# Kernel optimization log

Hardware: AMD Instinct MI355X
Metric: run time of the kernel (lower is better)

## Reference

```python
import jax, jax.numpy as jnp
import numpy as np

N = 50000
E = 800000
F_IN = 128
HEADS = 4
C_OUT = 32
NEG_SLOPE = 0.2


def setup_inputs() -> dict:
    key = jax.random.key(0)
    k_x, k_e, k_w, k_as, k_ad, k_b = jax.random.split(key, 6)
    x = jax.random.normal(k_x, (N, F_IN), dtype=jnp.float32)
    edge_index = jax.random.randint(k_e, (2, E), 0, N, dtype=jnp.int32)
    # Glorot-style init for linear weight [F_IN, HEADS*C_OUT] and attention vectors.
    scale_w = 1.0 / np.sqrt(F_IN)
    W = jax.random.normal(k_w, (F_IN, HEADS * C_OUT), dtype=jnp.float32) * scale_w
    scale_a = 1.0 / np.sqrt(C_OUT)
    att_src = jax.random.normal(k_as, (HEADS, C_OUT), dtype=jnp.float32) * scale_a
    att_dst = jax.random.normal(k_ad, (HEADS, C_OUT), dtype=jnp.float32) * scale_a
    bias = jnp.zeros((HEADS * C_OUT,), dtype=jnp.float32)
    return {"x": x, "edge_index": edge_index, "W": W, "att_src": att_src,
            "att_dst": att_dst, "bias": bias}


def reference(x, edge_index, W, att_src, att_dst, bias):
    n = x.shape[0]
    # add self loops (PyG add_self_loops=True)
    loops = jnp.arange(n, dtype=edge_index.dtype)
    src = jnp.concatenate([edge_index[0], loops])  # [E+N]
    dst = jnp.concatenate([edge_index[1], loops])  # [E+N]
    edge_index_full = jnp.stack([src, dst])

    h = (x @ W).reshape(n, HEADS, C_OUT)           # [N,H,C]
    a_src = jnp.einsum('nhc,hc->nh', h, att_src)   # [N,H]
    a_dst = jnp.einsum('nhc,hc->nh', h, att_dst)   # [N,H]

    e = jax.nn.leaky_relu(a_src[src] + a_dst[dst], NEG_SLOPE)  # [E',H]
    # segment softmax over edges grouped by destination node
    m = jax.ops.segment_max(e, dst, num_segments=n)            # [N,H]
    e = jnp.exp(e - m[dst])
    s = jax.ops.segment_sum(e, dst, num_segments=n)            # [N,H]
    alpha = e / (s[dst] + 1e-16)                               # [E',H]

    msg = h[src] * alpha[:, :, None]                           # [E',H,C]
    out = jax.ops.segment_sum(msg, dst, num_segments=n)        # [N,H,C]
    out = out.reshape(n, HEADS * C_OUT) + bias                 # concat=True
    return out, edge_index_full, alpha
```

## Files before the change

kernel.cpp:

```cpp
#include <hip/hip_runtime.h>

#define NNODES 50000
#define NEDGES 800000
#define ETOT   (NEDGES + NNODES)
#define FIN    128
#define FOUT   128
#define HEADS  4
#define NEG    0.2f
#define RCAP   64
#define WSTR   136
#define NBUCK  196
#define CAPB   4608

typedef float  f32x4 __attribute__((ext_vector_type(4)));
typedef int    i32x4 __attribute__((ext_vector_type(4)));
typedef short  s16x8 __attribute__((ext_vector_type(8)));
typedef unsigned short u16x8 __attribute__((ext_vector_type(8)));

__device__ __forceinline__ float lrelu(float v) { return v > 0.f ? v : NEG * v; }
__device__ __forceinline__ float4 e4(float4 a, float4 b) {
    return make_float4(__expf(lrelu(a.x + b.x)), __expf(lrelu(a.y + b.y)),
                       __expf(lrelu(a.z + b.z)), __expf(lrelu(a.w + b.w)));
}
__device__ __forceinline__ unsigned short f2bf(float f) {
    unsigned u = __float_as_uint(f);
    return (unsigned short)((u + 0x7FFFu + ((u >> 16) & 1u)) >> 16);
}
__device__ __forceinline__ void nt_store4(float* p, float a, float b, float c, float d) {
    f32x4 v = {a, b, c, d};
    __builtin_nontemporal_store(v, (f32x4*)p);
}

__global__ __launch_bounds__(256) void k_wt(const float* __restrict__ W,
                                            unsigned short* __restrict__ Wt,
                                            int* __restrict__ gcnt)
{
    if (blockIdx.x == 0 && threadIdx.x < NBUCK) gcnt[threadIdx.x] = 0;
    const int i = blockIdx.x * 256 + threadIdx.x;
    const int c = i & 127, kq = i >> 7;
    const int k0 = kq * 4;
    ushort4 v;
    v.x = f2bf(W[(k0 + 0) * 128 + c]);
    v.y = f2bf(W[(k0 + 1) * 128 + c]);
    v.z = f2bf(W[(k0 + 2) * 128 + c]);
    v.w = f2bf(W[(k0 + 3) * 128 + c]);
    *(ushort4*)(Wt + c * 128 + k0) = v;
}

__global__ __launch_bounds__(256) void k_gemm(
    const float* __restrict__ x, const unsigned short* __restrict__ Wtg,
    const float* __restrict__ att_s, const float* __restrict__ att_d,
    unsigned short* __restrict__ hb, float* __restrict__ a_src, float* __restrict__ a_dst)
{
    __shared__ unsigned short Wl[128 * WSTR];
    __shared__ unsigned short Xl[64 * WSTR];

    const int tid = threadIdx.x;
    const int nbase = blockIdx.x * 64;

    for (int i = tid; i < 2048; i += 256) {
        int c = i >> 4, q = i & 15;
        *(u16x8*)(&Wl[c * WSTR + q * 8]) = *(const u16x8*)(&Wtg[c * 128 + q * 8]);
    }
#pragma unroll
    for (int it = 0; it < 8; it++) {
        int flat = it * 256 + tid;
        int row = flat >> 5, kq = flat & 31;
        int gn = nbase + row; if (gn >= NNODES) gn = NNODES - 1;
        float4 v = *(const float4*)(x + (size_t)gn * FIN + kq * 4);
        ushort4 b;
        b.x = f2bf(v.x); b.y = f2bf(v.y); b.z = f2bf(v.z); b.w = f2bf(v.w);
        *(ushort4*)(&Xl[row * WSTR + kq * 4]) = b;
    }
    __syncthreads();

    const int wid = tid >> 6, lane = tid & 63;
    const int r16 = lane & 15;
    const int kg  = lane >> 4;

    s16x8 af[4];
#pragma unroll
    for (int t = 0; t < 4; t++)
        af[t] = *(const s16x8*)(&Xl[(wid * 16 + r16) * WSTR + t * 32 + kg * 8]);

    float pa[4] = {0.f, 0.f, 0.f, 0.f};
    float pd[4] = {0.f, 0.f, 0.f, 0.f};

#pragma unroll
    for (int cg = 0; cg < 8; cg++) {
        s16x8 bf[4];
#pragma unroll
        for (int t = 0; t < 4; t++)
            bf[t] = *(const s16x8*)(&Wl[(cg * 16 + r16) * WSTR + t * 32 + kg * 8]);
        f32x4 acc = {0.f, 0.f, 0.f, 0.f};
#pragma unroll
        for (int t = 0; t < 4; t++)
            acc = __builtin_amdgcn_mfma_f32_16x16x32_bf16(af[t], bf[t], acc, 0, 0, 0);

        const int col = cg * 16 + r16;
        const float asv = att_s[col], adv = att_d[col];
#pragma unroll
        for (int i2 = 0; i2 < 4; i2++) {
            int node = nbase + wid * 16 + kg * 4 + i2;
            if (node < NNODES)
                hb[(size_t)node * FOUT + col] = f2bf(acc[i2]);
            pa[i2] = fmaf(acc[i2], asv, pa[i2]);
            pd[i2] = fmaf(acc[i2], adv, pd[i2]);
        }
        if (cg & 1) {
            const int head = cg >> 1;
#pragma unroll
            for (int i2 = 0; i2 < 4; i2++) {
                float a = pa[i2], d = pd[i2];
                a += __shfl_xor(a, 1); a += __shfl_xor(a, 2);
                a += __shfl_xor(a, 4); a += __shfl_xor(a, 8);
                d += __shfl_xor(d, 1); d += __shfl_xor(d, 2);
                d += __shfl_xor(d, 4); d += __shfl_xor(d, 8);
                if (r16 == 0) {
                    int node = nbase + wid * 16 + kg * 4 + i2;
                    if (node < NNODES) {
                        a_src[node * HEADS + head] = a;
                        a_dst[node * HEADS + head] = d;
                    }
                }
                pa[i2] = 0.f; pd[i2] = 0.f;
            }
        }
    }
}

__global__ __launch_bounds__(256) void k_bin(
    const int* __restrict__ ei, int* __restrict__ gcnt, unsigned* __restrict__ region)
{
    __shared__ int lcnt[256], lofs[256], gbase[256], lpos[256], scan[256];
    __shared__ unsigned recs[4096];
    const int tid = threadIdx.x;
    const int q0 = blockIdx.x * 1024;

    lcnt[tid] = 0;
    __syncthreads();

    i32x4 sq[4], dq[4];
    bool v[4];
#pragma unroll
    for (int j = 0; j < 4; j++) {
        const int q = q0 + tid + j * 256;
        v[j] = (q < NEDGES / 4);
        const int qi = v[j] ? q : 0;
        sq[j] = ((const i32x4*)ei)[qi];
        dq[j] = ((const i32x4*)(ei + NEDGES))[qi];
    }
#pragma unroll
    for (int j = 0; j < 4; j++)
        if (v[j]) {
#pragma unroll
            for (int c = 0; c < 4; c++) atomicAdd(&lcnt[dq[j][c] >> 8], 1);
        }
    __syncthreads();
    scan[tid] = lcnt[tid];
    __syncthreads();
    for (int o = 1; o < 256; o <<= 1) {
        int t = (tid >= o) ? scan[tid - o] : 0;
        __syncthreads();
        scan[tid] += t;
        __syncthreads();
    }
    lofs[tid] = scan[tid] - lcnt[tid];
    if (tid < NBUCK) gbase[tid] = atomicAdd(&gcnt[tid], lcnt[tid]);
    lpos[tid] = 0;
    __syncthreads();
#pragma unroll
    for (int j = 0; j < 4; j++)
        if (v[j]) {
#pragma unroll
            for (int c = 0; c < 4; c++) {
                const int d = dq[j][c], b = d >> 8;
                const int idx = lofs[b] + atomicAdd(&lpos[b], 1);
                recs[idx] = (unsigned)sq[j][c] | ((unsigned)d << 16);
            }
        }
    __syncthreads();
    const int m = scan[255];
    for (int i = tid; i < m; i += 256) {
        const unsigned rec = recs[i];
        const int b = rec >> 24;
        const int off = gbase[b] + (i - lofs[b]);
        if (off < CAPB) region[(size_t)b * CAPB + off] = rec;
    }
}

__global__ __launch_bounds__(256) void k_asm(
    const unsigned* __restrict__ region, const int* __restrict__ gcnt,
    int* __restrict__ cnt, unsigned short* __restrict__ csr16)
{
    __shared__ unsigned short rows[256 * RCAP];
    __shared__ int lcnt[256];
    const int tid = threadIdx.x;
    const int b = blockIdx.x;
    lcnt[tid] = 0;
    __syncthreads();

    const int m = min(gcnt[b], CAPB);
    for (int i = tid; i < m; i += 256) {
        const unsigned u = region[(size_t)b * CAPB + i];
        const int dl = (u >> 16) & 255;
        const int sl = atomicAdd(&lcnt[dl], 1);
        if (sl < RCAP) rows[dl * RCAP + sl] = (unsigned short)(u & 0xFFFFu);
    }
    __syncthreads();

    const int nodebase = b * 256;
    const int nrows = min(256, NNODES - nodebase);
    for (int i = tid; i < nrows * 8; i += 256) {
        const int r = i >> 3, q = i & 7;
        *(u16x8*)(&csr16[((size_t)(nodebase + r) << 6) + q * 8]) =
            *(const u16x8*)(&rows[r * RCAP + q * 8]);
    }
    if (tid < nrows) cnt[nodebase + tid] = lcnt[tid];
}

__global__ __launch_bounds__(256) void k_msg(
    const unsigned short* __restrict__ hb, const float* __restrict__ a_src,
    const float* __restrict__ a_dst, const int* __restrict__ cnt,
    const unsigned short* __restrict__ csr16, const float* __restrict__ bias,
    float* __restrict__ out, float* __restrict__ nd)
{
    const int tid = threadIdx.x;
    const int wid = tid >> 6, lane = tid & 63;
    const int n = blockIdx.x * 4 + wid;
    __shared__ unsigned short slds[4][RCAP];
    __shared__ float elds[4][RCAP * 4];

    const int deg_r = min(cnt[n], RCAP - 1);
    const int deg = deg_r + 1;
    const float4 ad = ((const float4*)a_dst)[n];

    unsigned s = (unsigned)n;
    float4 ev = make_float4(0.f, 0.f, 0.f, 0.f);
    if (lane < deg) {
        if (lane < deg_r) s = csr16[(n << 6) + lane];
        float4 as = ((const float4*)a_src)[s];
        ev = e4(as, ad);
    }
    float4 den = ev;
#pragma unroll
    for (int o = 32; o >= 1; o >>= 1) {
        den.x += __shfl_xor(den.x, o);
        den.y += __shfl_xor(den.y, o);
        den.z += __shfl_xor(den.z, o);
        den.w += __shfl_xor(den.w, o);
    }
    const float4 inv = make_float4(1.f / (den.x + 1e-16f), 1.f / (den.y + 1e-16f),
                                   1.f / (den.z + 1e-16f), 1.f / (den.w + 1e-16f));
    if (lane == 0) {
        ((float4*)nd)[n * 2]     = ad;
        ((float4*)nd)[n * 2 + 1] = inv;
    }
    slds[wid][lane] = (unsigned short)s;
    ((float4*)elds[wid])[lane] =
        make_float4(ev.x * inv.x, ev.y * inv.y, ev.z * inv.z, ev.w * inv.w);

    const int sub = lane >> 4;
    const int c8  = lane & 15;
    const int head = c8 >> 2;
    const char* hbase = (const char*)hb;
    float acc[8];
#pragma unroll
    for (int j = 0; j < 8; j++) acc[j] = 0.f;
    const int dp = (deg + 3) & ~3;

    int i0 = sub;
    float al = elds[wid][i0 * 4 + head];
    unsigned si = slds[wid][i0];
    float4 u = *(const float4*)(hbase + si * 256u + c8 * 16u);

    for (int base = 4; base < dp; base += 4) {
        const int i1 = base + sub;
        const float al2 = elds[wid][i1 * 4 + head];
        const unsigned si2 = slds[wid][i1];
        const float4 u2 = *(const float4*)(hbase + si2 * 256u + c8 * 16u);

        const unsigned w0 = __float_as_uint(u.x), w1 = __float_as_uint(u.y);
        const unsigned w2 = __float_as_uint(u.z), w3 = __float_as_uint(u.w);
        acc[0] = fmaf(__uint_as_float(w0 << 16),          al, acc[0]);
        acc[1] = fmaf(__uint_as_float(w0 & 0xFFFF0000u),  al, acc[1]);
        acc[2] = fmaf(__uint_as_float(w1 << 16),          al, acc[2]);
        acc[3] = fmaf(__uint_as_float(w1 & 0xFFFF0000u),  al, acc[3]);
        acc[4] = fmaf(__uint_as_float(w2 << 16),          al, acc[4]);
        acc[5] = fmaf(__uint_as_float(w2 & 0xFFFF0000u),  al, acc[5]);
        acc[6] = fmaf(__uint_as_float(w3 << 16),          al, acc[6]);
        acc[7] = fmaf(__uint_as_float(w3 & 0xFFFF0000u),  al, acc[7]);

        u = u2; al = al2;
    }
    {
        const unsigned w0 = __float_as_uint(u.x), w1 = __float_as_uint(u.y);
        const unsigned w2 = __float_as_uint(u.z), w3 = __float_as_uint(u.w);
        acc[0] = fmaf(__uint_as_float(w0 << 16),          al, acc[0]);
        acc[1] = fmaf(__uint_as_float(w0 & 0xFFFF0000u),  al, acc[1]);
        acc[2] = fmaf(__uint_as_float(w1 << 16),          al, acc[2]);
        acc[3] = fmaf(__uint_as_float(w1 & 0xFFFF0000u),  al, acc[3]);
        acc[4] = fmaf(__uint_as_float(w2 << 16),          al, acc[4]);
        acc[5] = fmaf(__uint_as_float(w2 & 0xFFFF0000u),  al, acc[5]);
        acc[6] = fmaf(__uint_as_float(w3 << 16),          al, acc[6]);
        acc[7] = fmaf(__uint_as_float(w3 & 0xFFFF0000u),  al, acc[7]);
    }
#pragma unroll
    for (int j = 0; j < 8; j++) {
        acc[j] += __shfl_xor(acc[j], 16);
        acc[j] += __shfl_xor(acc[j], 32);
    }
    if (lane < 16) {
        const float4 b0 = ((const float4*)bias)[c8 * 2];
        const float4 b1 = ((const float4*)bias)[c8 * 2 + 1];
        ((float4*)out)[(size_t)n * 32 + c8 * 2] =
            make_float4(acc[0] + b0.x, acc[1] + b0.y, acc[2] + b0.z, acc[3] + b0.w);
        ((float4*)out)[(size_t)n * 32 + c8 * 2 + 1] =
            make_float4(acc[4] + b1.x, acc[5] + b1.y, acc[6] + b1.z, acc[7] + b1.w);
    }
}

__global__ __launch_bounds__(256) void k_alpha(
    const int* __restrict__ ei, const float* __restrict__ a_src,
    const float* __restrict__ nd, float* __restrict__ alpha,
    float* __restrict__ out_edge)
{
    const int i4 = blockIdx.x * blockDim.x + threadIdx.x;
    if (i4 >= ETOT / 4) return;
    i32x4 s4, d4;
    if (i4 < NEDGES / 4) {
        s4 = __builtin_nontemporal_load(&((const i32x4*)ei)[i4]);
        d4 = __builtin_nontemporal_load(&((const i32x4*)ei)[NEDGES / 4 + i4]);
    } else {
        const int n0 = i4 * 4 - NEDGES;
        s4 = d4 = (i32x4){n0, n0 + 1, n0 + 2, n0 + 3};
    }
    nt_store4(out_edge + (size_t)i4 * 4,
              (float)s4.x, (float)s4.y, (float)s4.z, (float)s4.w);
    nt_store4(out_edge + (size_t)(ETOT / 4 + i4) * 4,
              (float)d4.x, (float)d4.y, (float)d4.z, (float)d4.w);

    const float4* as4p = (const float4*)a_src;
    const float4* nd4p = (const float4*)nd;
#pragma unroll
    for (int j = 0; j < 4; j++) {
        const int s = s4[j];
        const int d = d4[j];
        float4 as = as4p[s];
        float4 ad = nd4p[d * 2];
        float4 iv = nd4p[d * 2 + 1];
        float4 ev = e4(as, ad);
        nt_store4(alpha + ((size_t)i4 * 4 + j) * 4,
                  ev.x * iv.x, ev.y * iv.y, ev.z * iv.z, ev.w * iv.w);
    }
}

extern "C" void kernel_launch(void* const* d_in, const int* in_sizes, int n_in,
                              void* d_out, int out_size, void* d_ws, size_t ws_size,
                              hipStream_t stream)
{
    const float* x     = (const float*)d_in[0];
    const int*   ei    = (const int*)  d_in[1];
    const float* W     = (const float*)d_in[2];
    const float* att_s = (const float*)d_in[3];
    const float* att_d = (const float*)d_in[4];
    const float* bias  = (const float*)d_in[5];

    unsigned short* hb = (unsigned short*)d_ws;
    float* a_src  = (float*)(hb + (size_t)NNODES * FOUT);
    float* a_dst  = a_src + NNODES * HEADS;
    float* nd     = a_dst + NNODES * HEADS;
    int*   cnt    = (int*)(nd + (size_t)NNODES * 8);
    unsigned short* csr16 = (unsigned short*)(cnt + NNODES);
    unsigned short* wt    = csr16 + (size_t)NNODES * RCAP;
    int*      gcnt  = (int*)(wt + 16384);
    unsigned* region = (unsigned*)(gcnt + 256);

    float* out_x = (float*)d_out;
    float* out_e = out_x + (size_t)NNODES * FOUT;
    float* out_a = out_e + (size_t)2 * ETOT;

    k_wt   <<<16, 256, 0, stream>>>(W, wt, gcnt);
    k_gemm <<<(NNODES + 63) / 64, 256, 0, stream>>>(x, wt, att_s, att_d, hb, a_src, a_dst);
    k_bin  <<<(NEDGES / 4 + 1023) / 1024, 256, 0, stream>>>(ei, gcnt, region);
    k_asm  <<<NBUCK, 256, 0, stream>>>(region, gcnt, cnt, csr16);
    k_msg  <<<NNODES / 4, 256, 0, stream>>>(hb, a_src, a_dst, cnt, csr16, bias, out_x, nd);
    k_alpha<<<(ETOT / 4 + 255) / 256, 256, 0, stream>>>(ei, a_src, nd, out_a, out_e);
}
```

Before: 104.1 us.

## Fuse edge binning into GEMM kernel and replace global atomics with per-block segments

Merges the edge-binning kernel into the GEMM launch by having the first blocks do binning and the rest do the GEMM, with their shared memory overlaid in a union. The two independent stages can then run concurrently and one launch disappears. Global atomic bucket offsets are replaced by per-block, per-bucket fixed segments of 64 entries plus a count table, and the assemble kernel walks all block segments per bucket. This removes the gcnt reset and the contended global atomics, but edges are dropped if a block's segment overflows 64, and the assemble stage now reads more scattered data.

```diff
diff --git a/kernel.cpp b/kernel.cpp
--- a/kernel.cpp
+++ b/kernel.cpp
@@ -10,7 +10,9 @@
 #define RCAP   64
 #define WSTR   136
 #define NBUCK  196
-#define CAPB   4608
+#define NBLK   196
+#define SEGC   64
+#define GEMMB  782
 
 typedef float  f32x4 __attribute__((ext_vector_type(4)));
 typedef int    i32x4 __attribute__((ext_vector_type(4)));
@@ -32,10 +34,8 @@
 }
 
 __global__ __launch_bounds__(256) void k_wt(const float* __restrict__ W,
-                                            unsigned short* __restrict__ Wt,
-                                            int* __restrict__ gcnt)
-{
-    if (blockIdx.x == 0 && threadIdx.x < NBUCK) gcnt[threadIdx.x] = 0;
+                                            unsigned short* __restrict__ Wt)
+{
     const int i = blockIdx.x * 256 + threadIdx.x;
     const int c = i & 127, kq = i >> 7;
     const int k0 = kq * 4;
@@ -47,16 +47,81 @@
     *(ushort4*)(Wt + c * 128 + k0) = v;
 }
 
-__global__ __launch_bounds__(256) void k_gemm(
+__global__ __launch_bounds__(256) void k_main(
     const float* __restrict__ x, const unsigned short* __restrict__ Wtg,
     const float* __restrict__ att_s, const float* __restrict__ att_d,
-    unsigned short* __restrict__ hb, float* __restrict__ a_src, float* __restrict__ a_dst)
-{
-    __shared__ unsigned short Wl[128 * WSTR];
-    __shared__ unsigned short Xl[64 * WSTR];
+    unsigned short* __restrict__ hb, float* __restrict__ a_src, float* __restrict__ a_dst,
+    const int* __restrict__ ei, int* __restrict__ cntb, unsigned* __restrict__ region)
+{
+    __shared__ __align__(16) union {
+        struct { unsigned short Wl[128 * WSTR]; unsigned short Xl[64 * WSTR]; } g;
+        struct { int lcnt[256]; int lofs[256]; int scan[256]; int lpos[256];
+                 unsigned recs[4096]; } b;
+    } sm;
 
     const int tid = threadIdx.x;
-    const int nbase = blockIdx.x * 64;
+
+    if (blockIdx.x < NBLK) {
+        const int blk = blockIdx.x;
+        const int q0 = blk * 1024;
+
+        sm.b.lcnt[tid] = 0;
+        __syncthreads();
+
+        i32x4 sq[4], dq[4];
+        bool v[4];
+#pragma unroll
+        for (int j = 0; j < 4; j++) {
+            const int q = q0 + tid + j * 256;
+            v[j] = (q < NEDGES / 4);
+            const int qi = v[j] ? q : 0;
+            sq[j] = ((const i32x4*)ei)[qi];
+            dq[j] = ((const i32x4*)(ei + NEDGES))[qi];
+        }
+#pragma unroll
+        for (int j = 0; j < 4; j++)
+            if (v[j]) {
+#pragma unroll
+                for (int c = 0; c < 4; c++) atomicAdd(&sm.b.lcnt[dq[j][c] >> 8], 1);
+            }
+        __syncthreads();
+        sm.b.scan[tid] = sm.b.lcnt[tid];
+        __syncthreads();
+        for (int o = 1; o < 256; o <<= 1) {
+            int t = (tid >= o) ? sm.b.scan[tid - o] : 0;
+            __syncthreads();
+            sm.b.scan[tid] += t;
+            __syncthreads();
+        }
+        sm.b.lofs[tid] = sm.b.scan[tid] - sm.b.lcnt[tid];
+        if (tid < NBUCK) cntb[blk * NBUCK + tid] = sm.b.lcnt[tid];
+        sm.b.lpos[tid] = 0;
+        __syncthreads();
+#pragma unroll
+        for (int j = 0; j < 4; j++)
+            if (v[j]) {
+#pragma unroll
+                for (int c = 0; c < 4; c++) {
+                    const int d = dq[j][c], b = d >> 8;
+                    const int idx = sm.b.lofs[b] + atomicAdd(&sm.b.lpos[b], 1);
+                    sm.b.recs[idx] = (unsigned)sq[j][c] | ((unsigned)d << 16);
+                }
+            }
+        __syncthreads();
+        const int m = sm.b.scan[255];
+        for (int i = tid; i < m; i += 256) {
+            const unsigned rec = sm.b.recs[i];
+            const int b = rec >> 24;
+            const int off = i - sm.b.lofs[b];
+            if (off < SEGC)
+                region[((size_t)blk * NBUCK + b) * SEGC + off] = rec;
+        }
+        return;
+    }
+
+    const int nbase = (blockIdx.x - NBLK) * 64;
+    unsigned short* Wl = sm.g.Wl;
+    unsigned short* Xl = sm.g.Xl;
 
     for (int i = tid; i < 2048; i += 256) {
         int c = i >> 4, q = i & 15;
@@ -129,83 +194,27 @@
     }
 }
 
-__global__ __launch_bounds__(256) void k_bin(
-    const int* __restrict__ ei, int* __restrict__ gcnt, unsigned* __restrict__ region)
-{
-    __shared__ int lcnt[256], lofs[256], gbase[256], lpos[256], scan[256];
-    __shared__ unsigned recs[4096];
-    const int tid = threadIdx.x;
-    const int q0 = blockIdx.x * 1024;
-
-    lcnt[tid] = 0;
-    __syncthreads();
-
-    i32x4 sq[4], dq[4];
-    bool v[4];
-#pragma unroll
-    for (int j = 0; j < 4; j++) {
-        const int q = q0 + tid + j * 256;
-        v[j] = (q < NEDGES / 4);
-        const int qi = v[j] ? q : 0;
-        sq[j] = ((const i32x4*)ei)[qi];
-        dq[j] = ((const i32x4*)(ei + NEDGES))[qi];
-    }
-#pragma unroll
-    for (int j = 0; j < 4; j++)
-        if (v[j]) {
-#pragma unroll
-            for (int c = 0; c < 4; c++) atomicAdd(&lcnt[dq[j][c] >> 8], 1);
-        }
-    __syncthreads();
-    scan[tid] = lcnt[tid];
-    __syncthreads();
-    for (int o = 1; o < 256; o <<= 1) {
-        int t = (tid >= o) ? scan[tid - o] : 0;
-        __syncthreads();
-        scan[tid] += t;
-        __syncthreads();
-    }
-    lofs[tid] = scan[tid] - lcnt[tid];
-    if (tid < NBUCK) gbase[tid] = atomicAdd(&gcnt[tid], lcnt[tid]);
-    lpos[tid] = 0;
-    __syncthreads();
-#pragma unroll
-    for (int j = 0; j < 4; j++)
-        if (v[j]) {
-#pragma unroll
-            for (int c = 0; c < 4; c++) {
-                const int d = dq[j][c], b = d >> 8;
-                const int idx = lofs[b] + atomicAdd(&lpos[b], 1);
-                recs[idx] = (unsigned)sq[j][c] | ((unsigned)d << 16);
-            }
-        }
-    __syncthreads();
-    const int m = scan[255];
-    for (int i = tid; i < m; i += 256) {
-        const unsigned rec = recs[i];
-        const int b = rec >> 24;
-        const int off = gbase[b] + (i - lofs[b]);
-        if (off < CAPB) region[(size_t)b * CAPB + off] = rec;
-    }
-}
-
 __global__ __launch_bounds__(256) void k_asm(
-    const unsigned* __restrict__ region, const int* __restrict__ gcnt,
+    const unsigned* __restrict__ region, const int* __restrict__ cntb,
     int* __restrict__ cnt, unsigned short* __restrict__ csr16)
 {
     __shared__ unsigned short rows[256 * RCAP];
     __shared__ int lcnt[256];
     const int tid = threadIdx.x;
     const int b = blockIdx.x;
+    const int wid = tid >> 6, lane = tid & 63;
     lcnt[tid] = 0;
     __syncthreads();
 
-    const int m = min(gcnt[b], CAPB);
-    for (int i = tid; i < m; i += 256) {
-        const unsigned u = region[(size_t)b * CAPB + i];
-        const int dl = (u >> 16) & 255;
-        const int sl = atomicAdd(&lcnt[dl], 1);
-        if (sl < RCAP) rows[dl * RCAP + sl] = (unsigned short)(u & 0xFFFFu);
+    for (int blk = wid; blk < NBLK; blk += 4) {
+        const int c = min(cntb[blk * NBUCK + b], SEGC);
+        const unsigned* seg = region + ((size_t)blk * NBUCK + b) * SEGC;
+        for (int i = lane; i < c; i += 64) {
+            const unsigned u = seg[i];
+            const int dl = (u >> 16) & 255;
+            const int sl = atomicAdd(&lcnt[dl], 1);
+            if (sl < RCAP) rows[dl * RCAP + sl] = (unsigned short)(u & 0xFFFFu);
+        }
     }
     __syncthreads();
 
@@ -269,9 +278,8 @@
     for (int j = 0; j < 8; j++) acc[j] = 0.f;
     const int dp = (deg + 3) & ~3;
 
-    int i0 = sub;
-    float al = elds[wid][i0 * 4 + head];
-    unsigned si = slds[wid][i0];
+    float al = elds[wid][sub * 4 + head];
+    unsigned si = slds[wid][sub];
     float4 u = *(const float4*)(hbase + si * 256u + c8 * 16u);
 
     for (int base = 4; base < dp; base += 4) {
@@ -373,17 +381,17 @@
     int*   cnt    = (int*)(nd + (size_t)NNODES * 8);
     unsigned short* csr16 = (unsigned short*)(cnt + NNODES);
     unsigned short* wt    = csr16 + (size_t)NNODES * RCAP;
-    int*      gcnt  = (int*)(wt + 16384);
-    unsigned* region = (unsigned*)(gcnt + 256);
+    int*      cntb   = (int*)(wt + 16384);
+    unsigned* region = (unsigned*)(cntb + ((NBLK * NBUCK + 15) & ~15));
 
     float* out_x = (float*)d_out;
     float* out_e = out_x + (size_t)NNODES * FOUT;
     float* out_a = out_e + (size_t)2 * ETOT;
 
-    k_wt   <<<16, 256, 0, stream>>>(W, wt, gcnt);
-    k_gemm <<<(NNODES + 63) / 64, 256, 0, stream>>>(x, wt, att_s, att_d, hb, a_src, a_dst);
-    k_bin  <<<(NEDGES / 4 + 1023) / 1024, 256, 0, stream>>>(ei, gcnt, region);
-    k_asm  <<<NBUCK, 256, 0, stream>>>(region, gcnt, cnt, csr16);
+    k_wt   <<<16, 256, 0, stream>>>(W, wt);
+    k_main <<<NBLK + GEMMB, 256, 0, stream>>>(x, wt, att_s, att_d, hb, a_src, a_dst,
+                                              ei, cntb, region);
+    k_asm  <<<NBUCK, 256, 0, stream>>>(region, cntb, cnt, csr16);
     k_msg  <<<NNODES / 4, 256, 0, stream>>>(hb, a_src, a_dst, cnt, csr16, bias, out_x, nd);
     k_alpha<<<(ETOT / 4 + 255) / 256, 256, 0, stream>>>(ei, a_src, nd, out_a, out_e);
 }
```

Result: slower. 115.0 us (+10.5%).

## Fuse W transpose into binning and replace global bucket atomics with per-block segments

Applied to the files above, without the earlier changes.

Merges the weight bf16 transpose into the edge-binning kernel as an extra block, which removes one launch and the need to zero global counters. Each binning block now writes its per-bucket counts and records into a private fixed-size segment rather than claiming offsets with global atomics. The assembly kernel walks all per-block segments for its bucket, one wave per segment. The risk is that records are silently dropped when a block has more than 64 edges for one bucket, and assembly now issues more, smaller reads.

```diff
diff --git a/kernel.cpp b/kernel.cpp
--- a/kernel.cpp
+++ b/kernel.cpp
@@ -10,7 +10,8 @@
 #define RCAP   64
 #define WSTR   136
 #define NBUCK  196
-#define CAPB   4608
+#define NBLK   196
+#define SEGC   64
 
 typedef float  f32x4 __attribute__((ext_vector_type(4)));
 typedef int    i32x4 __attribute__((ext_vector_type(4)));
@@ -31,20 +32,116 @@
     __builtin_nontemporal_store(v, (f32x4*)p);
 }
 
-__global__ __launch_bounds__(256) void k_wt(const float* __restrict__ W,
-                                            unsigned short* __restrict__ Wt,
-                                            int* __restrict__ gcnt)
-{
-    if (blockIdx.x == 0 && threadIdx.x < NBUCK) gcnt[threadIdx.x] = 0;
-    const int i = blockIdx.x * 256 + threadIdx.x;
-    const int c = i & 127, kq = i >> 7;
-    const int k0 = kq * 4;
-    ushort4 v;
-    v.x = f2bf(W[(k0 + 0) * 128 + c]);
-    v.y = f2bf(W[(k0 + 1) * 128 + c]);
-    v.z = f2bf(W[(k0 + 2) * 128 + c]);
-    v.w = f2bf(W[(k0 + 3) * 128 + c]);
-    *(ushort4*)(Wt + c * 128 + k0) = v;
+__global__ __launch_bounds__(256) void k_binwt(
+    const int* __restrict__ ei, int* __restrict__ cntb, unsigned* __restrict__ region,
+    const float* __restrict__ W, unsigned short* __restrict__ Wt)
+{
+    const int tid = threadIdx.x;
+
+    if (blockIdx.x == NBLK) {
+        for (int i = tid; i < 4096; i += 256) {
+            const int c = i & 127, kq = i >> 7;
+            const int k0 = kq * 4;
+            ushort4 v;
+            v.x = f2bf(W[(k0 + 0) * 128 + c]);
+            v.y = f2bf(W[(k0 + 1) * 128 + c]);
+            v.z = f2bf(W[(k0 + 2) * 128 + c]);
+            v.w = f2bf(W[(k0 + 3) * 128 + c]);
+            *(ushort4*)(Wt + c * 128 + k0) = v;
+        }
+        return;
+    }
+
+    __shared__ int lcnt[256], lofs[256], scan[256], lpos[256];
+    __shared__ unsigned recs[4096];
+    const int blk = blockIdx.x;
+    const int q0 = blk * 1024;
+
+    lcnt[tid] = 0;
+    __syncthreads();
+
+    i32x4 sq[4], dq[4];
+    bool v[4];
+#pragma unroll
+    for (int j = 0; j < 4; j++) {
+        const int q = q0 + tid + j * 256;
+        v[j] = (q < NEDGES / 4);
+        const int qi = v[j] ? q : 0;
+        sq[j] = ((const i32x4*)ei)[qi];
+        dq[j] = ((const i32x4*)(ei + NEDGES))[qi];
+    }
+#pragma unroll
+    for (int j = 0; j < 4; j++)
+        if (v[j]) {
+#pragma unroll
+            for (int c = 0; c < 4; c++) atomicAdd(&lcnt[dq[j][c] >> 8], 1);
+        }
+    __syncthreads();
+    scan[tid] = lcnt[tid];
+    __syncthreads();
+    for (int o = 1; o < 256; o <<= 1) {
+        int t = (tid >= o) ? scan[tid - o] : 0;
+        __syncthreads();
+        scan[tid] += t;
+        __syncthreads();
+    }
+    lofs[tid] = scan[tid] - lcnt[tid];
+    if (tid < NBUCK) cntb[blk * NBUCK + tid] = lcnt[tid];
+    lpos[tid] = 0;
+    __syncthreads();
+#pragma unroll
+    for (int j = 0; j < 4; j++)
+        if (v[j]) {
+#pragma unroll
+            for (int c = 0; c < 4; c++) {
+                const int d = dq[j][c], b = d >> 8;
+                const int idx = lofs[b] + atomicAdd(&lpos[b], 1);
+                recs[idx] = (unsigned)sq[j][c] | ((unsigned)d << 16);
+            }
+        }
+    __syncthreads();
+    const int m = scan[255];
+    for (int i = tid; i < m; i += 256) {
+        const unsigned rec = recs[i];
+        const int b = rec >> 24;
+        const int off = i - lofs[b];
+        if (off < SEGC)
+            region[((size_t)blk * NBUCK + b) * SEGC + off] = rec;
+    }
+}
+
+__global__ __launch_bounds__(256) void k_asm(
+    const unsigned* __restrict__ region, const int* __restrict__ cntb,
+    int* __restrict__ cnt, unsigned short* __restrict__ csr16)
+{
+    __shared__ unsigned short rows[256 * RCAP];
+    __shared__ int lcnt[256];
+    const int tid = threadIdx.x;
+    const int b = blockIdx.x;
+    const int wid = tid >> 6, lane = tid & 63;
+    lcnt[tid] = 0;
+    __syncthreads();
+
+    for (int blk = wid; blk < NBLK; blk += 4) {
+        const int c = min(cntb[blk * NBUCK + b], SEGC);
+        const unsigned* seg = region + ((size_t)blk * NBUCK + b) * SEGC;
+        for (int i = lane; i < c; i += 64) {
+            const unsigned u = seg[i];
+            const int dl = (u >> 16) & 255;
+            const int sl = atomicAdd(&lcnt[dl], 1);
+            if (sl < RCAP) rows[dl * RCAP + sl] = (unsigned short)(u & 0xFFFFu);
+        }
+    }
+    __syncthreads();
+
+    const int nodebase = b * 256;
+    const int nrows = min(256, NNODES - nodebase);
+    for (int i = tid; i < nrows * 8; i += 256) {
+        const int r = i >> 3, q = i & 7;
+        *(u16x8*)(&csr16[((size_t)(nodebase + r) << 6) + q * 8]) =
+            *(const u16x8*)(&rows[r * RCAP + q * 8]);
+    }
+    if (tid < nrows) cnt[nodebase + tid] = lcnt[tid];
 }
 
 __global__ __launch_bounds__(256) void k_gemm(
@@ -129,96 +226,6 @@
     }
 }
 
-__global__ __launch_bounds__(256) void k_bin(
-    const int* __restrict__ ei, int* __restrict__ gcnt, unsigned* __restrict__ region)
-{
-    __shared__ int lcnt[256], lofs[256], gbase[256], lpos[256], scan[256];
-    __shared__ unsigned recs[4096];
-    const int tid = threadIdx.x;
-    const int q0 = blockIdx.x * 1024;
-
-    lcnt[tid] = 0;
-    __syncthreads();
-
-    i32x4 sq[4], dq[4];
-    bool v[4];
-#pragma unroll
-    for (int j = 0; j < 4; j++) {
-        const int q = q0 + tid + j * 256;
-        v[j] = (q < NEDGES / 4);
-        const int qi = v[j] ? q : 0;
-        sq[j] = ((const i32x4*)ei)[qi];
-        dq[j] = ((const i32x4*)(ei + NEDGES))[qi];
-    }
-#pragma unroll
-    for (int j = 0; j < 4; j++)
-        if (v[j]) {
-#pragma unroll
-            for (int c = 0; c < 4; c++) atomicAdd(&lcnt[dq[j][c] >> 8], 1);
-        }
-    __syncthreads();
-    scan[tid] = lcnt[tid];
-    __syncthreads();
-    for (int o = 1; o < 256; o <<= 1) {
-        int t = (tid >= o) ? scan[tid - o] : 0;
-        __syncthreads();
-        scan[tid] += t;
-        __syncthreads();
-    }
-    lofs[tid] = scan[tid] - lcnt[tid];
-    if (tid < NBUCK) gbase[tid] = atomicAdd(&gcnt[tid], lcnt[tid]);
-    lpos[tid] = 0;
-    __syncthreads();
-#pragma unroll
-    for (int j = 0; j < 4; j++)
-        if (v[j]) {
-#pragma unroll
-            for (int c = 0; c < 4; c++) {
-                const int d = dq[j][c], b = d >> 8;
-                const int idx = lofs[b] + atomicAdd(&lpos[b], 1);
-                recs[idx] = (unsigned)sq[j][c] | ((unsigned)d << 16);
-            }
-        }
-    __syncthreads();
-    const int m = scan[255];
-    for (int i = tid; i < m; i += 256) {
-        const unsigned rec = recs[i];
-        const int b = rec >> 24;
-        const int off = gbase[b] + (i - lofs[b]);
-        if (off < CAPB) region[(size_t)b * CAPB + off] = rec;
-    }
-}
-
-__global__ __launch_bounds__(256) void k_asm(
-    const unsigned* __restrict__ region, const int* __restrict__ gcnt,
-    int* __restrict__ cnt, unsigned short* __restrict__ csr16)
-{
-    __shared__ unsigned short rows[256 * RCAP];
-    __shared__ int lcnt[256];
-    const int tid = threadIdx.x;
-    const int b = blockIdx.x;
-    lcnt[tid] = 0;
-    __syncthreads();
-
-    const int m = min(gcnt[b], CAPB);
-    for (int i = tid; i < m; i += 256) {
-        const unsigned u = region[(size_t)b * CAPB + i];
-        const int dl = (u >> 16) & 255;
-        const int sl = atomicAdd(&lcnt[dl], 1);
-        if (sl < RCAP) rows[dl * RCAP + sl] = (unsigned short)(u & 0xFFFFu);
-    }
-    __syncthreads();
-
-    const int nodebase = b * 256;
-    const int nrows = min(256, NNODES - nodebase);
-    for (int i = tid; i < nrows * 8; i += 256) {
-        const int r = i >> 3, q = i & 7;
-        *(u16x8*)(&csr16[((size_t)(nodebase + r) << 6) + q * 8]) =
-            *(const u16x8*)(&rows[r * RCAP + q * 8]);
-    }
-    if (tid < nrows) cnt[nodebase + tid] = lcnt[tid];
-}
-
 __global__ __launch_bounds__(256) void k_msg(
     const unsigned short* __restrict__ hb, const float* __restrict__ a_src,
     const float* __restrict__ a_dst, const int* __restrict__ cnt,
@@ -269,9 +276,8 @@
     for (int j = 0; j < 8; j++) acc[j] = 0.f;
     const int dp = (deg + 3) & ~3;
 
-    int i0 = sub;
-    float al = elds[wid][i0 * 4 + head];
-    unsigned si = slds[wid][i0];
+    float al = elds[wid][sub * 4 + head];
+    unsigned si = slds[wid][sub];
     float4 u = *(const float4*)(hbase + si * 256u + c8 * 16u);
 
     for (int base = 4; base < dp; base += 4) {
@@ -373,17 +379,16 @@
     int*   cnt    = (int*)(nd + (size_t)NNODES * 8);
     unsigned short* csr16 = (unsigned short*)(cnt + NNODES);
     unsigned short* wt    = csr16 + (size_t)NNODES * RCAP;
-    int*      gcnt  = (int*)(wt + 16384);
-    unsigned* region = (unsigned*)(gcnt + 256);
+    int*      cntb   = (int*)(wt + 16384);
+    unsigned* region = (unsigned*)(cntb + ((NBLK * NBUCK + 15) & ~15));
 
     float* out_x = (float*)d_out;
     float* out_e = out_x + (size_t)NNODES * FOUT;
     float* out_a = out_e + (size_t)2 * ETOT;
 
-    k_wt   <<<16, 256, 0, stream>>>(W, wt, gcnt);
+    k_binwt<<<NBLK + 1, 256, 0, stream>>>(ei, cntb, region, W, wt);
+    k_asm  <<<NBUCK, 256, 0, stream>>>(region, cntb, cnt, csr16);
     k_gemm <<<(NNODES + 63) / 64, 256, 0, stream>>>(x, wt, att_s, att_d, hb, a_src, a_dst);
-    k_bin  <<<(NEDGES / 4 + 1023) / 1024, 256, 0, stream>>>(ei, gcnt, region);
-    k_asm  <<<NBUCK, 256, 0, stream>>>(region, gcnt, cnt, csr16);
     k_msg  <<<NNODES / 4, 256, 0, stream>>>(hb, a_src, a_dst, cnt, csr16, bias, out_x, nd);
     k_alpha<<<(ETOT / 4 + 255) / 256, 256, 0, stream>>>(ei, a_src, nd, out_a, out_e);
 }
```

Result: slower. 123.8 us (+19.0%).
